# Kernel tuning notes

Hardware: AMD Instinct MI355X
Metric: run time of the kernel (lower is better)

The kernel has to match this reference:

```python
import jax, jax.numpy as jnp
import numpy as np
from jax import lax

B, N, C = 4, 3072, 512
SAMPLE_RATIO = 0.25
CLUSTER_NUM = int(np.ceil(N * SAMPLE_RATIO))  # 768, static (mask=None, no 'r')
K = 5  # self.k, since k <= cluster_num


def setup_inputs() -> dict:
    key = jax.random.key(0)
    k1, = jax.random.split(key, 1)
    x = jax.random.normal(k1, (B, N, C), dtype=jnp.float32)
    # idx_token starts as identity mapping per batch (standard TCFormer init)
    idx_token = jnp.tile(jnp.arange(N, dtype=jnp.int32)[None, :], (B, 1))
    agg_weight = jnp.ones((B, N, 1), dtype=jnp.float32)
    return {"x": x, "idx_token": idx_token, "agg_weight": agg_weight}


def _cluster_dpc_knn(x):
    # runs under no_grad in torch -> stop_gradient here
    xs = lax.stop_gradient(x).astype(jnp.float32)
    sq = jnp.sum(xs * xs, axis=-1)  # [B,N]
    d2 = sq[:, :, None] + sq[:, None, :] - 2.0 * jnp.einsum('bnc,bmc->bnm', xs, xs)
    dist = jnp.sqrt(jnp.maximum(d2, 0.0)) / jnp.sqrt(jnp.float32(C))  # cdist / C**0.5
    # k nearest (smallest) distances
    neg_nearest, _ = lax.top_k(-dist, K)
    dist_nearest = -neg_nearest  # [B,N,K]
    density = jnp.exp(-jnp.mean(dist_nearest ** 2, axis=-1))
    density = density + jax.random.uniform(jax.random.key(42), density.shape, dtype=density.dtype) * 1e-6
    mask = (density[:, None, :] > density[:, :, None]).astype(x.dtype)  # [B,N,N]
    dist_max = jnp.max(dist.reshape(B, -1), axis=-1)[:, None, None]
    dist_min = jnp.min(dist * mask + dist_max * (1.0 - mask), axis=-1)  # [B,N]
    score = dist_min * density
    _, index_down = lax.top_k(score, CLUSTER_NUM)  # [B,cluster]
    # gather rows of dist at cluster centers, assign each token to nearest center
    dmat = jnp.take_along_axis(dist, index_down[:, :, None], axis=1)  # [B,cluster,N]
    idx_cluster = jnp.argmin(dmat, axis=1).astype(jnp.int32)  # [B,N]
    # force centers to map to their own cluster id
    idx_cluster = idx_cluster.at[jnp.arange(B)[:, None], index_down].set(
        jnp.broadcast_to(jnp.arange(CLUSTER_NUM, dtype=jnp.int32)[None, :], (B, CLUSTER_NUM)))
    return idx_cluster


def reference(x, idx_token, agg_weight):
    idx_cluster = _cluster_dpc_knn(x)
    # merge_tokens
    token_weight = jnp.ones((B, N, 1), dtype=x.dtype)
    idx = idx_cluster + jnp.arange(B, dtype=jnp.int32)[:, None] * CLUSTER_NUM  # [B,N]
    idx_flat = idx.reshape(-1)
    all_weight = jax.ops.segment_sum(token_weight.reshape(-1), idx_flat,
                                     num_segments=B * CLUSTER_NUM) + 1e-6  # [B*cluster]
    norm_weight = token_weight / all_weight[idx_flat].reshape(B, N, 1)  # [B,N,1]
    x_merged = jax.ops.segment_sum((x * norm_weight).reshape(B * N, C), idx_flat,
                                   num_segments=B * CLUSTER_NUM).reshape(B, CLUSTER_NUM, C)
    idx_token_new = jnp.take_along_axis(idx_cluster, idx_token, axis=1)  # [B,N]
    weight_t = jnp.take_along_axis(norm_weight, idx_token[:, :, None], axis=1)  # [B,N,1]
    agg_weight_new = agg_weight * weight_t
    return x_merged, agg_weight_new, idx_token_new, idx_cluster
```

## Files before the change

kernel.cpp:

```cpp
#include <hip/hip_runtime.h>
#include <math.h>
#include <float.h>

constexpr int B  = 4;
constexpr int N  = 3072;
constexpr int C  = 512;
constexpr int CL = 768;

typedef unsigned short u16;
typedef __attribute__((ext_vector_type(8))) short s16x8;
typedef __attribute__((ext_vector_type(4))) float f32x4;

__device__ __forceinline__ unsigned rotl32(unsigned v, int d) { return (v << d) | (v >> (32 - d)); }

__device__ inline void threefry2x32(unsigned k0, unsigned k1, unsigned c0, unsigned c1,
                                    unsigned& o0, unsigned& o1) {
  unsigned ks0 = k0, ks1 = k1, ks2 = 0x1BD11BDAu ^ k0 ^ k1;
  unsigned x0 = c0 + ks0, x1 = c1 + ks1;
#define TF_RND(r) { x0 += x1; x1 = rotl32(x1, (r)); x1 ^= x0; }
  TF_RND(13) TF_RND(15) TF_RND(26) TF_RND(6)  x0 += ks1; x1 += ks2 + 1u;
  TF_RND(17) TF_RND(29) TF_RND(16) TF_RND(24) x0 += ks2; x1 += ks0 + 2u;
  TF_RND(13) TF_RND(15) TF_RND(26) TF_RND(6)  x0 += ks0; x1 += ks1 + 3u;
  TF_RND(17) TF_RND(29) TF_RND(16) TF_RND(24) x0 += ks1; x1 += ks2 + 4u;
  TF_RND(13) TF_RND(15) TF_RND(26) TF_RND(6)  x0 += ks2; x1 += ks0 + 5u;
#undef TF_RND
  o0 = x0; o1 = x1;
}

__device__ inline float jax_uniform_bn(int f) {
  constexpr int HALF = (B * N) / 2;
  unsigned o0, o1, bits;
  if (f < HALF) { threefry2x32(0u, 42u, (unsigned)f, (unsigned)(f + HALF), o0, o1); bits = o0; }
  else          { threefry2x32(0u, 42u, (unsigned)(f - HALF), (unsigned)f, o0, o1); bits = o1; }
  return __uint_as_float((bits >> 9) | 0x3f800000u) - 1.0f;
}

__global__ void k_init(int* counts, unsigned long long* packed) {
  int g = blockIdx.x * 256 + threadIdx.x;
  packed[g] = ~0ull;
  if (g < B * CL) counts[g] = 0;
}

__global__ __launch_bounds__(64) void k_sq(const float* __restrict__ x, float* __restrict__ sq) {
  int row = blockIdx.x;
  int lane = threadIdx.x;
  const float* xr = x + (size_t)row * C;
  float s = 0.f;
  for (int c = lane * 4; c < C; c += 256) {
    float4 v = *(const float4*)(xr + c);
    s += v.x * v.x + v.y * v.y + v.z * v.z + v.w * v.w;
  }
  for (int o = 32; o > 0; o >>= 1) s += __shfl_down(s, o, 64);
  if (lane == 0) sq[row] = s;
}

__device__ __forceinline__ u16 bf16rn(float f) {
  unsigned u = __float_as_uint(f);
  unsigned r = u + 0x7FFFu + ((u >> 16) & 1u);
  return (u16)(r >> 16);
}
__device__ __forceinline__ float bf16tof(u16 h) {
  return __uint_as_float(((unsigned)h) << 16);
}

__global__ void k_split(const float* __restrict__ x, u16* __restrict__ xhi, u16* __restrict__ xlo) {
  int g = (blockIdx.x * 256 + threadIdx.x) * 4;
  float4 v = *(const float4*)(x + g);
  u16 h0 = bf16rn(v.x), h1 = bf16rn(v.y), h2 = bf16rn(v.z), h3 = bf16rn(v.w);
  u16 l0 = bf16rn(v.x - bf16tof(h0));
  u16 l1 = bf16rn(v.y - bf16tof(h1));
  u16 l2 = bf16rn(v.z - bf16tof(h2));
  u16 l3 = bf16rn(v.w - bf16tof(h3));
  uint2 hp, lp;
  hp.x = (unsigned)h0 | ((unsigned)h1 << 16); hp.y = (unsigned)h2 | ((unsigned)h3 << 16);
  lp.x = (unsigned)l0 | ((unsigned)l1 << 16); lp.y = (unsigned)l2 | ((unsigned)l3 << 16);
  *(uint2*)(xhi + g) = hp;
  *(uint2*)(xlo + g) = lp;
}

constexpr int NT3 = N / 128;
constexpr int NTILE3 = NT3 * (NT3 + 1) / 2;

__global__ __launch_bounds__(256) void k_distm(const u16* __restrict__ xhi, const u16* __restrict__ xlo,
                                               const float* __restrict__ sq,
                                               float* __restrict__ distbuf, int b0) {
  constexpr int ASTR = 40;
  __shared__ __align__(16) char smem[40960];
  u16* sAh = (u16*)smem;
  u16* sAl = sAh + 128 * ASTR;
  u16* sBh = sAl + 128 * ASTR;
  u16* sBl = sBh + 128 * ASTR;

  int bl = blockIdx.y, b = b0 + bl;
  int idx = blockIdx.x;
  int ti = 0, rem = idx;
  while (rem >= NT3 - ti) { rem -= NT3 - ti; ++ti; }
  int tj = ti + rem;
  int i0 = ti * 128, j0 = tj * 128;
  bool do_mirror = (ti != tj);

  const float* sqb = sq + (size_t)b * N;
  float* dist = distbuf + (size_t)bl * N * N;

  int tid = threadIdx.x;
  int srow = tid >> 1, shalf = (tid & 1) * 16;
  const u16* gAh = xhi + ((size_t)b * N + i0 + srow) * C + shalf;
  const u16* gAl = xlo + ((size_t)b * N + i0 + srow) * C + shalf;
  const u16* gBh = xhi + ((size_t)b * N + j0 + srow) * C + shalf;
  const u16* gBl = xlo + ((size_t)b * N + j0 + srow) * C + shalf;
  int wofs = srow * ASTR + shalf;

  int lane = tid & 63, w = tid >> 6;
  int wr = (w >> 1) * 64, wc = (w & 1) * 64;
  int l15 = lane & 15, l4 = lane >> 4;

  f32x4 acc[4][4];
#pragma unroll
  for (int rt = 0; rt < 4; ++rt)
#pragma unroll
    for (int ct = 0; ct < 4; ++ct)
#pragma unroll
      for (int e = 0; e < 4; ++e) acc[rt][ct][e] = 0.f;

  uint4 p0 = *(const uint4*)gAh, p1 = *(const uint4*)(gAh + 8);
  uint4 p2 = *(const uint4*)gAl, p3 = *(const uint4*)(gAl + 8);
  uint4 p4 = *(const uint4*)gBh, p5 = *(const uint4*)(gBh + 8);
  uint4 p6 = *(const uint4*)gBl, p7 = *(const uint4*)(gBl + 8);

  for (int k0 = 0; k0 < C; k0 += 32) {
    *(uint4*)&sAh[wofs] = p0; *(uint4*)&sAh[wofs + 8] = p1;
    *(uint4*)&sAl[wofs] = p2; *(uint4*)&sAl[wofs + 8] = p3;
    *(uint4*)&sBh[wofs] = p4; *(uint4*)&sBh[wofs + 8] = p5;
    *(uint4*)&sBl[wofs] = p6; *(uint4*)&sBl[wofs + 8] = p7;
    __syncthreads();
    int kn = k0 + 32;
    if (kn < C) {
      p0 = *(const uint4*)(gAh + kn); p1 = *(const uint4*)(gAh + kn + 8);
      p2 = *(const uint4*)(gAl + kn); p3 = *(const uint4*)(gAl + kn + 8);
      p4 = *(const uint4*)(gBh + kn); p5 = *(const uint4*)(gBh + kn + 8);
      p6 = *(const uint4*)(gBl + kn); p7 = *(const uint4*)(gBl + kn + 8);
    }
    s16x8 ah[4], al[4];
#pragma unroll
    for (int rt = 0; rt < 4; ++rt) {
      int ro = (wr + rt * 16 + l15) * ASTR + l4 * 8;
      ah[rt] = *(const s16x8*)&sAh[ro];
      al[rt] = *(const s16x8*)&sAl[ro];
    }
#pragma unroll
    for (int ct = 0; ct < 4; ++ct) {
      int co = (wc + ct * 16 + l15) * ASTR + l4 * 8;
      s16x8 bh = *(const s16x8*)&sBh[co];
      s16x8 bl = *(const s16x8*)&sBl[co];
#pragma unroll
      for (int rt = 0; rt < 4; ++rt) {
        acc[rt][ct] = __builtin_amdgcn_mfma_f32_16x16x32_bf16(ah[rt], bh, acc[rt][ct], 0, 0, 0);
        acc[rt][ct] = __builtin_amdgcn_mfma_f32_16x16x32_bf16(ah[rt], bl, acc[rt][ct], 0, 0, 0);
        acc[rt][ct] = __builtin_amdgcn_mfma_f32_16x16x32_bf16(al[rt], bh, acc[rt][ct], 0, 0, 0);
      }
    }
    __syncthreads();
  }

  const float SQC = 22.627416997969522f;
  float sqi[4][4], sqj[4];
#pragma unroll
  for (int rt = 0; rt < 4; ++rt)
#pragma unroll
    for (int r = 0; r < 4; ++r) sqi[rt][r] = sqb[i0 + wr + rt * 16 + l4 * 4 + r];
#pragma unroll
  for (int ct = 0; ct < 4; ++ct) sqj[ct] = sqb[j0 + wc + ct * 16 + l15];

#pragma unroll
  for (int rt = 0; rt < 4; ++rt)
#pragma unroll
    for (int ct = 0; ct < 4; ++ct)
#pragma unroll
      for (int r = 0; r < 4; ++r) {
        float d2 = fmaxf(sqi[rt][r] + sqj[ct] - 2.0f * acc[rt][ct][r], 0.0f);
        acc[rt][ct][r] = sqrtf(d2) / SQC;
      }

  constexpr int TSTR = 76;
  float* sT = (float*)smem + w * (32 * TSTR);

#pragma unroll
  for (int p = 0; p < 2; ++p) {
#pragma unroll
    for (int cth = 0; cth < 2; ++cth) {
      int ct = p * 2 + cth;
      int cl = cth * 16 + l15;
#pragma unroll
      for (int rt = 0; rt < 4; ++rt)
#pragma unroll
        for (int r = 0; r < 4; ++r)
          sT[cl * TSTR + rt * 16 + l4 * 4 + r] = acc[rt][ct][r];
    }
    {
      int g4 = lane & 7, rbase = lane >> 3;
#pragma unroll
      for (int it = 0; it < 8; ++it) {
        int rl = it * 8 + rbase;
        float4 v = make_float4(sT[(4 * g4 + 0) * TSTR + rl],
                               sT[(4 * g4 + 1) * TSTR + rl],
                               sT[(4 * g4 + 2) * TSTR + rl],
                               sT[(4 * g4 + 3) * TSTR + rl]);
        *(float4*)(dist + (size_t)(i0 + wr + rl) * N + j0 + wc + p * 32 + 4 * g4) = v;
      }
    }
    if (do_mirror) {
      int cg = lane >> 4, rq = lane & 15;
#pragma unroll
      for (int cc = 0; cc < 8; ++cc) {
        int c = cc * 4 + cg;
        float4 v = *(const float4*)&sT[c * TSTR + rq * 4];
        *(float4*)(dist + (size_t)(j0 + wc + p * 32 + c) * N + i0 + wr + rq * 4) = v;
      }
    }
  }
}

__device__ __forceinline__ void ins5b(float t[5], float v) {
  float c = v;
  float n;
  n = fminf(t[0], c); c = fmaxf(t[0], c); t[0] = n;
  n = fminf(t[1], c); c = fmaxf(t[1], c); t[1] = n;
  n = fminf(t[2], c); c = fmaxf(t[2], c); t[2] = n;
  n = fminf(t[3], c); c = fmaxf(t[3], c); t[3] = n;
  t[4] = fminf(t[4], c);
}

__global__ __launch_bounds__(256) void k_knn(const float* __restrict__ distbuf,
                                             float* __restrict__ density,
                                             float* __restrict__ rowmax, int b0) {
  int wv = threadIdx.x >> 6, lane = threadIdx.x & 63;
  int i = blockIdx.x * 4 + wv;
  int bl = blockIdx.y, b = b0 + bl;
  const float* row = distbuf + ((size_t)bl * N + i) * N;

  float t5[5] = {FLT_MAX, FLT_MAX, FLT_MAX, FLT_MAX, FLT_MAX};
  float mx = 0.f;
#pragma unroll
  for (int it = 0; it < N / 256; ++it) {
    float4 v = *(const float4*)(row + it * 256 + lane * 4);
    mx = fmaxf(mx, fmaxf(fmaxf(v.x, v.y), fmaxf(v.z, v.w)));
    ins5b(t5, v.x); ins5b(t5, v.y); ins5b(t5, v.z); ins5b(t5, v.w);
  }
#pragma unroll
  for (int m = 1; m < 64; m <<= 1) {
    mx = fmaxf(mx, __shfl_xor(mx, m, 64));
    float o0 = __shfl_xor(t5[0], m, 64);
    float o1 = __shfl_xor(t5[1], m, 64);
    float o2 = __shfl_xor(t5[2], m, 64);
    float o3 = __shfl_xor(t5[3], m, 64);
    float o4 = __shfl_xor(t5[4], m, 64);
    ins5b(t5, o0); ins5b(t5, o1); ins5b(t5, o2); ins5b(t5, o3); ins5b(t5, o4);
  }
  if (lane == 0) {
    float sum = t5[0] * t5[0] + t5[1] * t5[1] + t5[2] * t5[2] + t5[3] * t5[3] + t5[4] * t5[4];
    float dens = expf(-(sum / 5.0f)) + jax_uniform_bn(b * N + i) * 1e-6f;
    density[b * N + i] = dens;
    rowmax[b * N + i] = mx;
  }
}

__global__ __launch_bounds__(1024) void k_dmax(const float* __restrict__ rowmax,
                                               float* __restrict__ distmax) {
  __shared__ float red[16];
  int b = blockIdx.x;
  int tid = threadIdx.x;
  const float* rb = rowmax + (size_t)b * N;
  float mx = 0.f;
  for (int j = tid; j < N; j += 1024) mx = fmaxf(mx, rb[j]);
#pragma unroll
  for (int m = 1; m < 64; m <<= 1) mx = fmaxf(mx, __shfl_xor(mx, m, 64));
  if ((tid & 63) == 0) red[tid >> 6] = mx;
  __syncthreads();
  if (tid == 0) {
    float r = red[0];
#pragma unroll
    for (int q = 1; q < 16; ++q) r = fmaxf(r, red[q]);
    distmax[b] = r;
  }
}

__global__ __launch_bounds__(256) void k_maskmin(const float* __restrict__ distbuf,
                                                 const float* __restrict__ density,
                                                 const float* __restrict__ distmax,
                                                 float* __restrict__ score, int b0) {
  __shared__ float sd[N];
  int tid = threadIdx.x;
  int wv = tid >> 6, lane = tid & 63;
  int i = blockIdx.x * 4 + wv;
  int bl = blockIdx.y, b = b0 + bl;
  const float* db = density + (size_t)b * N;
  for (int j = tid * 4; j < N; j += 1024) *(float4*)(sd + j) = *(const float4*)(db + j);
  __syncthreads();
  float di = sd[i];
  float dmax = distmax[b];
  const float* row = distbuf + ((size_t)bl * N + i) * N;
  float mn = dmax;
#pragma unroll
  for (int it = 0; it < N / 256; ++it) {
    int j = it * 256 + lane * 4;
    float4 v = *(const float4*)(row + j);
    float4 d = *(const float4*)(sd + j);
    mn = fminf(mn, (d.x > di) ? v.x : dmax);
    mn = fminf(mn, (d.y > di) ? v.y : dmax);
    mn = fminf(mn, (d.z > di) ? v.z : dmax);
    mn = fminf(mn, (d.w > di) ? v.w : dmax);
  }
#pragma unroll
  for (int m = 1; m < 64; m <<= 1) mn = fminf(mn, __shfl_xor(mn, m, 64));
  if (lane == 0) score[b * N + i] = mn * di;
}

__global__ __launch_bounds__(256) void k_rank(const float* __restrict__ score,
                                              int* __restrict__ index_down,
                                              int* __restrict__ rank, int b0) {
  __shared__ float ssc[N];
  int tid = threadIdx.x;
  int wv = tid >> 6, lane = tid & 63;
  int i = blockIdx.x * 4 + wv;
  int b = b0 + blockIdx.y;
  const float* sb = score + (size_t)b * N;
  for (int j = tid * 4; j < N; j += 1024) *(float4*)(ssc + j) = *(const float4*)(sb + j);
  __syncthreads();
  float si = ssc[i];
  int cnt = 0;
#pragma unroll
  for (int it = 0; it < N / 256; ++it) {
    int j = it * 256 + lane * 4;
    float4 v = *(const float4*)(ssc + j);
    cnt += (v.x > si) || (v.x == si && (j + 0) < i);
    cnt += (v.y > si) || (v.y == si && (j + 1) < i);
    cnt += (v.z > si) || (v.z == si && (j + 2) < i);
    cnt += (v.w > si) || (v.w == si && (j + 3) < i);
  }
#pragma unroll
  for (int m = 1; m < 64; m <<= 1) cnt += __shfl_xor(cnt, m, 64);
  if (lane == 0) {
    rank[b * N + i] = (cnt < CL) ? cnt : -1;
    if (cnt < CL) index_down[b * CL + cnt] = i;
  }
}

__global__ __launch_bounds__(256) void k_assign_part(const float* __restrict__ distbuf,
                                                     const int* __restrict__ index_down,
                                                     unsigned long long* __restrict__ packed, int b0) {
  constexpr int RCH = CL / 8;
  __shared__ int sid[RCH];
  int bl = blockIdx.z, b = b0 + bl;
  int r0 = blockIdx.y * RCH;
  int tid = threadIdx.x;
  for (int r = tid; r < RCH; r += 256) sid[r] = index_down[b * CL + r0 + r];
  __syncthreads();
  int j = blockIdx.x * 256 + tid;
  const float* base = distbuf + (size_t)bl * N * N;
  float best = FLT_MAX; int bestr = 0;
#pragma unroll 8
  for (int r = 0; r < RCH; ++r) {
    float d = base[(size_t)sid[r] * N + j];
    if (d < best) { best = d; bestr = r0 + r; }
  }
  unsigned long long key = ((unsigned long long)__float_as_uint(best) << 32) | (unsigned)bestr;
  atomicMin(&packed[b * N + j], key);
}

__global__ void k_assign_fin2(const unsigned long long* __restrict__ packed,
                              const int* __restrict__ rank,
                              int* __restrict__ idx_cluster, int* __restrict__ counts) {
  int g = blockIdx.x * 256 + threadIdx.x;
  int b = g / N;
  int r = rank[g];
  int cl = (r >= 0) ? r : (int)(unsigned)(packed[g] & 0xffffffffull);
  idx_cluster[g] = cl;
  atomicAdd(&counts[b * CL + cl], 1);
}

__global__ __launch_bounds__(1024) void k_scan(const int* __restrict__ counts,
                                               int* __restrict__ offsets, int* __restrict__ cursor) {
  constexpr int T = B * CL;
  __shared__ int sm[T];
  int tid = threadIdx.x;
  for (int p = tid; p < T; p += 1024) sm[p] = counts[p];
  __syncthreads();
  for (int off = 1; off < T; off <<= 1) {
    int v[3]; int n = 0;
    for (int p = tid; p < T; p += 1024) { v[n++] = (p >= off) ? sm[p - off] : 0; }
    __syncthreads();
    n = 0;
    for (int p = tid; p < T; p += 1024) { sm[p] += v[n++]; }
    __syncthreads();
  }
  for (int p = tid; p < T; p += 1024) {
    int e = sm[p] - counts[p];
    offsets[p] = e; cursor[p] = e;
  }
}

__global__ void k_fill(const int* __restrict__ idx_cluster, int* __restrict__ cursor,
                       int* __restrict__ members) {
  int g = blockIdx.x * 256 + threadIdx.x;
  int b = g / N, i = g % N;
  int seg = b * CL + idx_cluster[g];
  int pos = atomicAdd(&cursor[seg], 1);
  members[pos] = i;
}

__global__ __launch_bounds__(128) void k_gather(const float* __restrict__ x, const int* __restrict__ members,
                                                const int* __restrict__ offsets, const int* __restrict__ counts,
                                                float* __restrict__ out0) {
  int seg = blockIdx.x;
  int b = seg / CL;
  int cnt = counts[seg], off = offsets[seg];
  float nw = 1.0f / ((float)cnt + 1e-6f);
  int c = threadIdx.x * 4;
  const float* xb = x + (size_t)b * N * C;
  float4 acc = make_float4(0.f, 0.f, 0.f, 0.f);
  for (int m = 0; m < cnt; ++m) {
    int tok = members[off + m];
    float4 v = *(const float4*)(xb + (size_t)tok * C + c);
    acc.x += v.x * nw; acc.y += v.y * nw; acc.z += v.z * nw; acc.w += v.w * nw;
  }
  *(float4*)(out0 + (size_t)seg * C + c) = acc;
}

__global__ void k_final(const float* __restrict__ agg_weight, const int* __restrict__ idx_token,
                        const int* __restrict__ idx_cluster, const int* __restrict__ counts,
                        float* __restrict__ out1, float* __restrict__ out2, float* __restrict__ out3) {
  int g = blockIdx.x * 256 + threadIdx.x;
  int b = g / N;
  int it = idx_token[g];
  int clt = idx_cluster[b * N + it];
  float nwt = 1.0f / ((float)counts[b * CL + clt] + 1e-6f);
  out1[g] = agg_weight[g] * nwt;
  out2[g] = (float)clt;
  out3[g] = (float)idx_cluster[g];
}

extern "C" void kernel_launch(void* const* d_in, const int* in_sizes, int n_in,
                              void* d_out, int out_size, void* d_ws, size_t ws_size,
                              hipStream_t stream) {
  const float* x          = (const float*)d_in[0];
  const int*   idx_token  = (const int*)d_in[1];
  const float* agg_weight = (const float*)d_in[2];

  float* out0 = (float*)d_out;
  float* out1 = out0 + (size_t)B * CL * C;
  float* out2 = out1 + (size_t)B * N;
  float* out3 = out2 + (size_t)B * N;

  char* w = (char*)d_ws;
  auto carve = [&](size_t bytes) { char* p = w; w += (bytes + 255) & ~(size_t)255; return p; };
  float*    sq         = (float*)carve((size_t)B * N * 4);
  float*    density    = (float*)carve((size_t)B * N * 4);
  float*    score      = (float*)carve((size_t)B * N * 4);
  float*    rowmax     = (float*)carve((size_t)B * N * 4);
  float*    distmax    = (float*)carve((size_t)B * 4);
  int*      index_down = (int*)carve((size_t)B * CL * 4);
  int*      rank       = (int*)carve((size_t)B * N * 4);
  int*      idx_clus   = (int*)carve((size_t)B * N * 4);
  int*      counts     = (int*)carve((size_t)B * CL * 4);
  int*      offsets    = (int*)carve((size_t)B * CL * 4);
  int*      cursor     = (int*)carve((size_t)B * CL * 4);
  int*      members    = (int*)carve((size_t)B * N * 4);
  unsigned long long* packed = (unsigned long long*)carve((size_t)B * N * 8);
  u16*      xhi        = (u16*)carve((size_t)B * N * C * 2);
  u16*      xlo        = (u16*)carve((size_t)B * N * C * 2);
  size_t used = (size_t)(w - (char*)d_ws);
  size_t per  = (size_t)N * N * 4;
  int nb_max = (ws_size > used) ? (int)((ws_size - used) / per) : 0;
  if (nb_max < 1) nb_max = 1;
  if (nb_max > B) nb_max = B;
  float* distbuf = (float*)w;

  k_init<<<(B * N) / 256, 256, 0, stream>>>(counts, packed);
  k_sq<<<B * N, 64, 0, stream>>>(x, sq);
  k_split<<<(B * N * C) / 1024, 256, 0, stream>>>(x, xhi, xlo);

  for (int b0 = 0; b0 < B; b0 += nb_max) {
    int nb = (B - b0 < nb_max) ? (B - b0) : nb_max;
    k_distm<<<dim3(NTILE3, nb), 256, 0, stream>>>(xhi, xlo, sq, distbuf, b0);
    k_knn<<<dim3(N / 4, nb), 256, 0, stream>>>(distbuf, density, rowmax, b0);
    k_dmax<<<nb, 1024, 0, stream>>>(rowmax + (size_t)b0 * N, distmax + b0);
    k_maskmin<<<dim3(N / 4, nb), 256, 0, stream>>>(distbuf, density, distmax, score, b0);
    k_rank<<<dim3(N / 4, nb), 256, 0, stream>>>(score, index_down, rank, b0);
    k_assign_part<<<dim3(N / 256, 8, nb), 256, 0, stream>>>(distbuf, index_down, packed, b0);
  }

  k_assign_fin2<<<(B * N) / 256, 256, 0, stream>>>(packed, rank, idx_clus, counts);
  k_scan<<<1, 1024, 0, stream>>>(counts, offsets, cursor);
  k_fill<<<(B * N) / 256, 256, 0, stream>>>(idx_clus, cursor, members);
  k_gather<<<B * CL, 128, 0, stream>>>(x, members, offsets, counts, out0);
  k_final<<<(B * N) / 256, 256, 0, stream>>>(agg_weight, idx_token, idx_clus, counts, out1, out2, out3);
}
```

Measured before the change: 308.6 us.

## Fuse kNN top-5 and row max into distance tile epilogue

Computes per-tile partial top-5 smallest distances and row maxima inside the distance-matrix kernel, for both the tile and its mirrored transpose. It writes these into a small partial buffer that a new lightweight kernel reduces into density and row max. This removes a full pass that reread the N×N distance matrix. The cost is extra serial insertion work and LDS reads in the distance kernel's epilogue, plus a new workspace buffer.

```diff
diff --git a/kernel.cpp b/kernel.cpp
--- a/kernel.cpp
+++ b/kernel.cpp
@@ -78,12 +78,23 @@
   *(uint2*)(xlo + g) = lp;
 }
 
+__device__ __forceinline__ void ins5b(float t[5], float v) {
+  float c = v;
+  float n;
+  n = fminf(t[0], c); c = fmaxf(t[0], c); t[0] = n;
+  n = fminf(t[1], c); c = fmaxf(t[1], c); t[1] = n;
+  n = fminf(t[2], c); c = fmaxf(t[2], c); t[2] = n;
+  n = fminf(t[3], c); c = fmaxf(t[3], c); t[3] = n;
+  t[4] = fminf(t[4], c);
+}
+
 constexpr int NT3 = N / 128;
 constexpr int NTILE3 = NT3 * (NT3 + 1) / 2;
 
 __global__ __launch_bounds__(256) void k_distm(const u16* __restrict__ xhi, const u16* __restrict__ xlo,
                                                const float* __restrict__ sq,
-                                               float* __restrict__ distbuf, int b0) {
+                                               float* __restrict__ distbuf,
+                                               float* __restrict__ part5, int b0) {
   constexpr int ASTR = 40;
   __shared__ __align__(16) char smem[40960];
   u16* sAh = (u16*)smem;
@@ -184,6 +195,9 @@
   constexpr int TSTR = 76;
   float* sT = (float*)smem + w * (32 * TSTR);
 
+  float t5A[5] = {FLT_MAX, FLT_MAX, FLT_MAX, FLT_MAX, FLT_MAX};
+  float mxA = 0.f;
+
 #pragma unroll
   for (int p = 0; p < 2; ++p) {
 #pragma unroll
@@ -217,51 +231,66 @@
         *(float4*)(dist + (size_t)(j0 + wc + p * 32 + c) * N + i0 + wr + rq * 4) = v;
       }
     }
-  }
-}
-
-__device__ __forceinline__ void ins5b(float t[5], float v) {
-  float c = v;
-  float n;
-  n = fminf(t[0], c); c = fmaxf(t[0], c); t[0] = n;
-  n = fminf(t[1], c); c = fmaxf(t[1], c); t[1] = n;
-  n = fminf(t[2], c); c = fmaxf(t[2], c); t[2] = n;
-  n = fminf(t[3], c); c = fmaxf(t[3], c); t[3] = n;
-  t[4] = fminf(t[4], c);
-}
-
-__global__ __launch_bounds__(256) void k_knn(const float* __restrict__ distbuf,
-                                             float* __restrict__ density,
-                                             float* __restrict__ rowmax, int b0) {
-  int wv = threadIdx.x >> 6, lane = threadIdx.x & 63;
-  int i = blockIdx.x * 4 + wv;
-  int bl = blockIdx.y, b = b0 + bl;
-  const float* row = distbuf + ((size_t)bl * N + i) * N;
-
+    for (int c = 0; c < 32; ++c) {
+      float v = sT[c * TSTR + lane];
+      mxA = fmaxf(mxA, v);
+      ins5b(t5A, v);
+    }
+    if (do_mirror) {
+      int cl = lane & 31, half = lane >> 5;
+      float t5B[5] = {FLT_MAX, FLT_MAX, FLT_MAX, FLT_MAX, FLT_MAX};
+      float mxB = 0.f;
+      for (int k = 0; k < 32; ++k) {
+        float v = sT[cl * TSTR + half * 32 + k];
+        mxB = fmaxf(mxB, v);
+        ins5b(t5B, v);
+      }
+      mxB = fmaxf(mxB, __shfl_xor(mxB, 32, 64));
+      float o0 = __shfl_xor(t5B[0], 32, 64);
+      float o1 = __shfl_xor(t5B[1], 32, 64);
+      float o2 = __shfl_xor(t5B[2], 32, 64);
+      float o3 = __shfl_xor(t5B[3], 32, 64);
+      float o4 = __shfl_xor(t5B[4], 32, 64);
+      ins5b(t5B, o0); ins5b(t5B, o1); ins5b(t5B, o2); ins5b(t5B, o3); ins5b(t5B, o4);
+      if (half == 0) {
+        int rowB = j0 + wc + p * 32 + cl;
+        int slotB = ti * 2 + (wr >> 6);
+        float* dst = part5 + (((size_t)bl * 48 + slotB) * 6) * N + rowB;
+        dst[0] = t5B[0]; dst[(size_t)N] = t5B[1]; dst[2 * (size_t)N] = t5B[2];
+        dst[3 * (size_t)N] = t5B[3]; dst[4 * (size_t)N] = t5B[4]; dst[5 * (size_t)N] = mxB;
+      }
+    }
+  }
+  {
+    int rowA = i0 + wr + lane;
+    int slotA = tj * 2 + (wc >> 6);
+    float* dst = part5 + (((size_t)bl * 48 + slotA) * 6) * N + rowA;
+    dst[0] = t5A[0]; dst[(size_t)N] = t5A[1]; dst[2 * (size_t)N] = t5A[2];
+    dst[3 * (size_t)N] = t5A[3]; dst[4 * (size_t)N] = t5A[4]; dst[5 * (size_t)N] = mxA;
+  }
+}
+
+__global__ __launch_bounds__(256) void k_dens(const float* __restrict__ part5,
+                                              float* __restrict__ density,
+                                              float* __restrict__ rowmax, int b0) {
+  int g = blockIdx.x * 256 + threadIdx.x;
+  int bl = g / N, r = g % N;
+  int b = b0 + bl;
+  const float* base = part5 + (size_t)bl * 48 * 6 * N + r;
   float t5[5] = {FLT_MAX, FLT_MAX, FLT_MAX, FLT_MAX, FLT_MAX};
   float mx = 0.f;
-#pragma unroll
-  for (int it = 0; it < N / 256; ++it) {
-    float4 v = *(const float4*)(row + it * 256 + lane * 4);
-    mx = fmaxf(mx, fmaxf(fmaxf(v.x, v.y), fmaxf(v.z, v.w)));
-    ins5b(t5, v.x); ins5b(t5, v.y); ins5b(t5, v.z); ins5b(t5, v.w);
-  }
-#pragma unroll
-  for (int m = 1; m < 64; m <<= 1) {
-    mx = fmaxf(mx, __shfl_xor(mx, m, 64));
-    float o0 = __shfl_xor(t5[0], m, 64);
-    float o1 = __shfl_xor(t5[1], m, 64);
-    float o2 = __shfl_xor(t5[2], m, 64);
-    float o3 = __shfl_xor(t5[3], m, 64);
-    float o4 = __shfl_xor(t5[4], m, 64);
-    ins5b(t5, o0); ins5b(t5, o1); ins5b(t5, o2); ins5b(t5, o3); ins5b(t5, o4);
-  }
-  if (lane == 0) {
-    float sum = t5[0] * t5[0] + t5[1] * t5[1] + t5[2] * t5[2] + t5[3] * t5[3] + t5[4] * t5[4];
-    float dens = expf(-(sum / 5.0f)) + jax_uniform_bn(b * N + i) * 1e-6f;
-    density[b * N + i] = dens;
-    rowmax[b * N + i] = mx;
-  }
+  for (int s = 0; s < 48; ++s) {
+    const float* sp = base + (size_t)s * 6 * N;
+    ins5b(t5, sp[0]);
+    ins5b(t5, sp[(size_t)N]);
+    ins5b(t5, sp[2 * (size_t)N]);
+    ins5b(t5, sp[3 * (size_t)N]);
+    ins5b(t5, sp[4 * (size_t)N]);
+    mx = fmaxf(mx, sp[5 * (size_t)N]);
+  }
+  float sum = t5[0] * t5[0] + t5[1] * t5[1] + t5[2] * t5[2] + t5[3] * t5[3] + t5[4] * t5[4];
+  density[b * N + r] = expf(-(sum / 5.0f)) + jax_uniform_bn(b * N + r) * 1e-6f;
+  rowmax[b * N + r] = mx;
 }
 
 __global__ __launch_bounds__(1024) void k_dmax(const float* __restrict__ rowmax,
@@ -468,6 +497,7 @@
   unsigned long long* packed = (unsigned long long*)carve((size_t)B * N * 8);
   u16*      xhi        = (u16*)carve((size_t)B * N * C * 2);
   u16*      xlo        = (u16*)carve((size_t)B * N * C * 2);
+  float*    part5      = (float*)carve((size_t)B * 48 * 6 * N * 4);
   size_t used = (size_t)(w - (char*)d_ws);
   size_t per  = (size_t)N * N * 4;
   int nb_max = (ws_size > used) ? (int)((ws_size - used) / per) : 0;
@@ -481,8 +511,8 @@
 
   for (int b0 = 0; b0 < B; b0 += nb_max) {
     int nb = (B - b0 < nb_max) ? (B - b0) : nb_max;
-    k_distm<<<dim3(NTILE3, nb), 256, 0, stream>>>(xhi, xlo, sq, distbuf, b0);
-    k_knn<<<dim3(N / 4, nb), 256, 0, stream>>>(distbuf, density, rowmax, b0);
+    k_distm<<<dim3(NTILE3, nb), 256, 0, stream>>>(xhi, xlo, sq, distbuf, part5, b0);
+    k_dens<<<(nb * N) / 256, 256, 0, stream>>>(part5, density, rowmax, b0);
     k_dmax<<<nb, 1024, 0, stream>>>(rowmax + (size_t)b0 * N, distmax + b0);
     k_maskmin<<<dim3(N / 4, nb), 256, 0, stream>>>(distbuf, density, distmax, score, b0);
     k_rank<<<dim3(N / 4, nb), 256, 0, stream>>>(score, index_down, rank, b0);
```

Measured after the change: 307.1 us. No clear change (-0.5%).
